# Kernel tuning notes

Measured on AMD Instinct MI355X. Metric: run time of the kernel, lower is better.

The kernel has to match this reference:

```python
import jax, jax.numpy as jnp
import numpy as np

D_MODEL = 1024
NUM_HEADS = 16
D_K = D_MODEL // NUM_HEADS
THETA = 10000.0


def _rope(x, cos, sin):
    # x: [b, h, l, d_k]; cos/sin: [l, d_k//2]
    x1 = x[..., ::2]
    x2 = x[..., 1::2]
    re = x1 * cos - x2 * sin
    ro = x1 * sin + x2 * cos
    return jnp.stack([re, ro], axis=-1).reshape(x.shape)


def setup_inputs() -> dict:
    key = jax.random.key(0)
    k0, k1, k2, k3, k4 = jax.random.split(key, 5)
    b, l = 2, 2048
    scale = 1.0 / np.sqrt(D_MODEL)
    return {
        "in_features": jax.random.normal(k0, (b, l, D_MODEL), dtype=jnp.float32),
        "wq": jax.random.normal(k1, (D_MODEL, D_MODEL), dtype=jnp.float32) * scale,
        "wk": jax.random.normal(k2, (D_MODEL, D_MODEL), dtype=jnp.float32) * scale,
        "wv": jax.random.normal(k3, (D_MODEL, D_MODEL), dtype=jnp.float32) * scale,
        "wo": jax.random.normal(k4, (D_MODEL, D_MODEL), dtype=jnp.float32) * scale,
    }


def reference(in_features, wq, wk, wv, wo):
    b, l, d = in_features.shape
    h, dk = NUM_HEADS, D_K

    def proj(w):
        # torch: einsum('b l d, k d -> b l k') == x @ w.T
        y = jnp.einsum('bld,kd->blk', in_features, w)
        return y.reshape(b, l, h, dk).transpose(0, 2, 1, 3)  # [b,h,l,dk]

    Q, K, V = proj(wq), proj(wk), proj(wv)

    # RoPE (use_rope=True)
    inv_freq = 1.0 / (THETA ** (jnp.arange(0, dk, 2, dtype=jnp.float32) / dk))
    angles = jnp.arange(l, dtype=jnp.float32)[:, None] * inv_freq[None, :]  # [l, dk//2]
    cos, sin = jnp.cos(angles), jnp.sin(angles)
    Q = _rope(Q, cos, sin)
    K = _rope(K, cos, sin)

    scores = jnp.einsum('bhqd,bhkd->bhqk', Q, K) / jnp.sqrt(jnp.float32(dk))
    causal = jnp.tril(jnp.ones((l, l), dtype=bool))  # [l,l]
    scores = jnp.where(causal[None, None], scores, jnp.float32(-jnp.inf))
    attn = jax.nn.softmax(scores, axis=-1)
    ctx = jnp.einsum('bhqk,bhkd->bhqd', attn, V)
    ctx = ctx.transpose(0, 2, 1, 3).reshape(b, l, d)  # [b,l,d_model]
    out = jnp.einsum('bld,md->blm', ctx, wo)
    return out
```

## Files before the change

### kernel.cpp

```cpp
#include <hip/hip_runtime.h>
#include <stdint.h>

typedef __attribute__((ext_vector_type(8))) short short8;
typedef __attribute__((ext_vector_type(4))) float floatx4;
typedef __attribute__((ext_vector_type(16))) float floatx16;

#define DEV static __device__ __forceinline__

DEV unsigned short f2bf(float f) {
  union { float f; uint32_t u; } v; v.f = f;
  return (unsigned short)((v.u + 0x7FFFu + ((v.u >> 16) & 1u)) >> 16);
}
DEV float bf2f(unsigned short h) {
  union { uint32_t u; float f; } v; v.u = ((uint32_t)h) << 16;
  return v.f;
}
DEV uint32_t cvtpk(float lo, float hi) {
  uint32_t d;
  asm("v_cvt_pk_bf16_f32 %0, %1, %2" : "=v"(d) : "v"(lo), "v"(hi));
  return d;
}
DEV void gload_lds16(const void* g, void* l) {
  __builtin_amdgcn_global_load_lds(
      (const __attribute__((address_space(1))) uint32_t*)g,
      (__attribute__((address_space(3))) uint32_t*)l, 16, 0, 0);
}

#if defined(__has_builtin)
#if __has_builtin(__builtin_amdgcn_permlane32_swap)
#define HAVE_PLSWAP 1
#endif
#endif
DEV void plswap(uint32_t& a, uint32_t& b) {
#ifdef HAVE_PLSWAP
  typedef unsigned int u2v __attribute__((ext_vector_type(2)));
  u2v r = __builtin_amdgcn_permlane32_swap(a, b, false, false);
  a = r.x; b = r.y;
#else
  uint32_t sa = (uint32_t)__shfl_xor((int)a, 32);
  uint32_t sb = (uint32_t)__shfl_xor((int)b, 32);
  uint32_t lane = __lane_id();
  uint32_t na = lane < 32 ? a : sb;
  uint32_t nb = lane < 32 ? sa : b;
  a = na; b = nb;
#endif
}
DEV float xmax32(float x) {
  union { float f; uint32_t u; } a, b; a.f = x; b.f = x;
  plswap(a.u, b.u);
  return fmaxf(a.f, b.f);
}
DEV float xsum32(float x) {
  union { float f; uint32_t u; } a, b; a.f = x; b.f = x;
  plswap(a.u, b.u);
  return a.f + b.f;
}

__global__ __launch_bounds__(256) void k_convert(
    const float* __restrict__ X, const float* __restrict__ Wq,
    const float* __restrict__ Wk, const float* __restrict__ Wv,
    const float* __restrict__ Wo, unsigned short* __restrict__ out) {
  long gid = (long)blockIdx.x * 256 + threadIdx.x;
  long e = gid * 8;
  int seg = (int)(e >> 20);
  const float* src; long base;
  if (seg < 4)      { src = X;  base = 0; }
  else if (seg == 4){ src = Wq; base = 4l << 20; }
  else if (seg == 5){ src = Wk; base = 5l << 20; }
  else if (seg == 6){ src = Wv; base = 6l << 20; }
  else              { src = Wo; base = 7l << 20; }
  const float4* s4 = (const float4*)(src + (e - base));
  float4 a = s4[0], b = s4[1];
  union { uint4 q; unsigned short s[8]; } u;
  u.s[0] = f2bf(a.x); u.s[1] = f2bf(a.y); u.s[2] = f2bf(a.z); u.s[3] = f2bf(a.w);
  u.s[4] = f2bf(b.x); u.s[5] = f2bf(b.y); u.s[6] = f2bf(b.z); u.s[7] = f2bf(b.w);
  *(uint4*)(out + e) = u.q;
}

template <int MODE>
__global__ __launch_bounds__(256) void k_gemm(
    const unsigned short* __restrict__ A,
    const unsigned short* __restrict__ B0, const unsigned short* __restrict__ B1,
    const unsigned short* __restrict__ B2,
    unsigned short* __restrict__ Qo, unsigned short* __restrict__ Ko,
    unsigned short* __restrict__ VFo, float* __restrict__ Cf, int K) {
  constexpr int MI = (MODE == 1) ? 2 : 4;
  constexpr int BM = MI * 32;
  __shared__ unsigned short At[BM * 64];
  __shared__ unsigned short Bt[128 * 64];
  const int tid = threadIdx.x, lane = tid & 63, wid = tid >> 6;
  const int wm = (wid >> 1) * (MI * 16), wn = (wid & 1) * 64;
  const int g = lane >> 4, c0 = lane & 15;
  const int bm0 = blockIdx.x * BM;
  const int bnG = blockIdx.y * 128;
  const unsigned short* Bp;
  int bn0;
  if constexpr (MODE == 0) {
    int wsel = bnG >> 10;
    Bp = wsel == 0 ? B0 : (wsel == 1 ? B1 : B2);
    bn0 = bnG & 1023;
  } else { Bp = B0; bn0 = bnG; }
  floatx4 acc[MI][4] = {};
  const int nk = K >> 6;
  const int koff = (blockIdx.x + blockIdx.y * 3) & (nk - 1);
  const int swzr = (c0 & 7) << 4;
  for (int s = 0; s < nk; ++s) {
    const int kt = ((s + koff) & (nk - 1)) << 6;
#pragma unroll
    for (int i = 0; i < MI; ++i) {
      int o = tid * 16 + i * 4096;
      int row = o >> 7;
      int col = (o & 127) ^ ((row & 7) << 4);
      gload_lds16((const char*)A + ((long)(bm0 + row) * K + kt + (col >> 1)) * 2, (char*)At + o);
    }
#pragma unroll
    for (int i = 0; i < 4; ++i) {
      int o = tid * 16 + i * 4096;
      int row = o >> 7;
      int col = (o & 127) ^ ((row & 7) << 4);
      gload_lds16((const char*)Bp + ((long)(bn0 + row) * K + kt + (col >> 1)) * 2, (char*)Bt + o);
    }
    __syncthreads();
#pragma unroll
    for (int kk = 0; kk < 2; ++kk) {
      const int kb = kk * 64 + g * 16;
      short8 av[MI], bv[4];
#pragma unroll
      for (int mi = 0; mi < MI; ++mi)
        av[mi] = *(const short8*)((const char*)At + (wm + mi * 16 + c0) * 128 + (kb ^ swzr));
#pragma unroll
      for (int ni = 0; ni < 4; ++ni)
        bv[ni] = *(const short8*)((const char*)Bt + (wn + ni * 16 + c0) * 128 + (kb ^ swzr));
#pragma unroll
      for (int mi = 0; mi < MI; ++mi)
#pragma unroll
        for (int ni = 0; ni < 4; ++ni)
          acc[mi][ni] = __builtin_amdgcn_mfma_f32_16x16x32_bf16(av[mi], bv[ni], acc[mi][ni], 0, 0, 0);
    }
    __syncthreads();
  }
  if constexpr (MODE == 1) {
#pragma unroll
    for (int mi = 0; mi < MI; ++mi)
#pragma unroll
      for (int ni = 0; ni < 4; ++ni)
#pragma unroll
        for (int i = 0; i < 4; ++i) {
          int r = bm0 + wm + mi * 16 + 4 * g + i;
          int cg = bnG + wn + ni * 16 + c0;
          Cf[(long)r * 1024 + cg] = acc[mi][ni][i];
        }
  } else {
    const int wsel = bnG >> 10;
#pragma unroll
    for (int mi = 0; mi < MI; ++mi)
#pragma unroll
      for (int ni = 0; ni < 4; ++ni)
#pragma unroll
        for (int i = 0; i < 4; ++i) {
          int r = bm0 + wm + mi * 16 + 4 * g + i;
          int cg = bnG + wn + ni * 16 + c0;
          int cc = cg & 1023, head = cc >> 6, dkk = cc & 63;
          int bb = r >> 11, ll = r & 2047;
          long bh = bb * 16 + head;
          float v = acc[mi][ni][i];
          if (wsel == 2) {
            int T = ll >> 6, rt = ll & 63;
            int m = rt >> 4, hb = (rt >> 3) & 1, j = rt & 7;
            int dvs = dkk >> 5, c = dkk & 31;
            VFo[bh * 131072 + T * 4096 + (dvs * 4 + m) * 512 + (hb * 32 + c) * 8 + j] = f2bf(v);
          } else {
            unsigned short* dst = wsel == 0 ? Qo : Ko;
            dst[(bh * 2048 + ll) * 64 + dkk] = f2bf(v);
          }
        }
  }
}

__global__ __launch_bounds__(256) void k_ropeQK(
    unsigned short* __restrict__ Qd, const unsigned short* __restrict__ Kin,
    unsigned short* __restrict__ KF, float qscale) {
  const int blk = blockIdx.x;
  const int tid = threadIdx.x;
  if (blk < 512) {
    int gid = blk * 256 + tid;
    int row = gid >> 1, hf = gid & 1;
    int l = row & 2047;
    unsigned short* p = Qd + (long)row * 64 + hf * 32;
    union { uint4 q[4]; unsigned short s[32]; } u;
#pragma unroll
    for (int i = 0; i < 4; ++i) u.q[i] = ((const uint4*)p)[i];
    float lf = (float)l;
#pragma unroll
    for (int j = 0; j < 16; ++j) {
      int pp = hf * 16 + j;
      float ang = lf * exp2f(-(float)pp * 0.4152410118609203f);
      float sv, cv; sincosf(ang, &sv, &cv);
      float x1 = bf2f(u.s[2 * j]), x2 = bf2f(u.s[2 * j + 1]);
      u.s[2 * j]     = f2bf((x1 * cv - x2 * sv) * qscale);
      u.s[2 * j + 1] = f2bf((x1 * sv + x2 * cv) * qscale);
    }
#pragma unroll
    for (int i = 0; i < 4; ++i) ((uint4*)p)[i] = u.q[i];
  } else {
    const int kblk = blk - 512;
    const int bh = kblk >> 5, T = kblk & 31;
    const unsigned short* src = Kin + ((long)bh * 2048 + T * 64) * 64;
    unsigned short* dst = KF + (long)kblk * 4096;
#pragma unroll
    for (int it = 0; it < 2; ++it) {
      int u = tid + it * 256;
      int lane = u & 63, kd = u >> 6;
      int kvs = kd >> 2, dseg = kd & 3;
      int row = kvs * 32 + (lane & 31);
      int col = dseg * 16 + 8 * (lane >> 5);
      union { uint4 q; unsigned short s[8]; } v;
      v.q = *(const uint4*)(src + row * 64 + col);
      float lf = (float)(T * 64 + row);
#pragma unroll
      for (int j = 0; j < 4; ++j) {
        int p = (col >> 1) + j;
        float ang = lf * exp2f(-(float)p * 0.4152410118609203f);
        float sv, cv; sincosf(ang, &sv, &cv);
        float x1 = bf2f(v.s[2 * j]), x2 = bf2f(v.s[2 * j + 1]);
        v.s[2 * j]     = f2bf(x1 * cv - x2 * sv);
        v.s[2 * j + 1] = f2bf(x1 * sv + x2 * cv);
      }
      *(uint4*)(dst + u * 8) = v.q;
    }
  }
}

DEV void attn_tile(int T, int Tend, int ntm1, int qabs, int h, int c,
                   const unsigned short* __restrict__ kfbase,
                   const unsigned short* __restrict__ vfbase,
                   const short8 (&qf)[4],
                   const short8 (&kc0)[4], const short8 (&kc1)[4],
                   short8 (&kn0)[4], short8 (&kn1)[4],
                   floatx16& ctx0, floatx16& ctx1, float& m_, float& l_) {
  {
    const int Tn = T + 1 < Tend ? T + 1 : T;
    const unsigned short* kt = kfbase + (long)Tn * 4096;
#pragma unroll
    for (int d = 0; d < 4; ++d) kn0[d] = *(const short8*)(kt + d * 512);
#pragma unroll
    for (int d = 0; d < 4; ++d) kn1[d] = *(const short8*)(kt + 2048 + d * 512);
  }
  const unsigned short* vt = vfbase + (long)T * 4096;
  short8 vf0[4], vf1[4];
#pragma unroll
  for (int m = 0; m < 4; ++m) vf0[m] = *(const short8*)(vt + m * 512);
#pragma unroll
  for (int m = 0; m < 4; ++m) vf1[m] = *(const short8*)(vt + 2048 + m * 512);

  floatx16 s0 = {}, s1 = {};
#pragma unroll
  for (int d = 0; d < 4; ++d)
    s0 = __builtin_amdgcn_mfma_f32_32x32x16_bf16(kc0[d], qf[d], s0, 0, 0, 0);
#pragma unroll
  for (int d = 0; d < 4; ++d)
    s1 = __builtin_amdgcn_mfma_f32_32x32x16_bf16(kc1[d], qf[d], s1, 0, 0, 0);

  if (T == ntm1) {
    const int kvb = T * 64 + 4 * h;
#pragma unroll
    for (int r = 0; r < 16; ++r) {
      const int off = (r & 3) + 8 * (r >> 2);
      if (kvb + off > qabs) s0[r] = -1e30f;
      if (kvb + 32 + off > qabs) s1[r] = -1e30f;
    }
  }
  float a4[8];
#pragma unroll
  for (int j = 0; j < 4; ++j) {
    a4[j]     = fmaxf(fmaxf(s0[4 * j], s0[4 * j + 1]), fmaxf(s0[4 * j + 2], s0[4 * j + 3]));
    a4[4 + j] = fmaxf(fmaxf(s1[4 * j], s1[4 * j + 1]), fmaxf(s1[4 * j + 2], s1[4 * j + 3]));
  }
  float mx = fmaxf(fmaxf(fmaxf(a4[0], a4[1]), fmaxf(a4[2], a4[3])),
                   fmaxf(fmaxf(a4[4], a4[5]), fmaxf(a4[6], a4[7])));
  mx = xmax32(mx);
  if (!__all(mx <= m_ + 8.0f)) {
    float mn = fmaxf(m_, mx);
    float sc = exp2f(m_ - mn);
    m_ = mn;
    l_ *= sc;
#pragma unroll
    for (int r = 0; r < 16; ++r) { ctx0[r] *= sc; ctx1[r] *= sc; }
  }
#pragma unroll
  for (int r = 0; r < 16; ++r) s0[r] = exp2f(s0[r] - m_);
#pragma unroll
  for (int r = 0; r < 16; ++r) s1[r] = exp2f(s1[r] - m_);
  float b4[8];
#pragma unroll
  for (int j = 0; j < 4; ++j) {
    b4[j]     = (s0[4 * j] + s0[4 * j + 1]) + (s0[4 * j + 2] + s0[4 * j + 3]);
    b4[4 + j] = (s1[4 * j] + s1[4 * j + 1]) + (s1[4 * j + 2] + s1[4 * j + 3]);
  }
  float rs = ((b4[0] + b4[1]) + (b4[2] + b4[3])) + ((b4[4] + b4[5]) + (b4[6] + b4[7]));
  rs = xsum32(rs);
  l_ += rs;

  uint32_t pd0[8], pd1[8];
#pragma unroll
  for (int d = 0; d < 8; ++d) {
    pd0[d] = cvtpk(s0[2 * d], s0[2 * d + 1]);
    pd1[d] = cvtpk(s1[2 * d], s1[2 * d + 1]);
  }
#pragma unroll
  for (int kvs = 0; kvs < 2; ++kvs) {
    const uint32_t* pd = kvs ? pd1 : pd0;
#pragma unroll
    for (int ks = 0; ks < 2; ++ks) {
      uint32_t u0 = pd[4 * ks], u2 = pd[4 * ks + 2];
      uint32_t u1 = pd[4 * ks + 1], u3 = pd[4 * ks + 3];
      plswap(u0, u2);
      plswap(u1, u3);
      union { uint32_t u[4]; short8 s; } bu;
      bu.u[0] = u0; bu.u[1] = u1; bu.u[2] = u2; bu.u[3] = u3;
      ctx0 = __builtin_amdgcn_mfma_f32_32x32x16_bf16(vf0[kvs * 2 + ks], bu.s, ctx0, 0, 0, 0);
      ctx1 = __builtin_amdgcn_mfma_f32_32x32x16_bf16(vf1[kvs * 2 + ks], bu.s, ctx1, 0, 0, 0);
    }
  }
}

__global__ __launch_bounds__(128) void k_attn(
    const unsigned short* __restrict__ Q, const unsigned short* __restrict__ KF,
    const unsigned short* __restrict__ VF, unsigned short* __restrict__ O) {
  __shared__ float lctx[64][33];
  __shared__ float lml[64][2];
  const int bid = blockIdx.x;
  const int xcd = bid & 7, idx = bid >> 3;
  const int head = idx >> 6;
  const int a = idx & 63;
  const int qs = (head < 2) ? a : 63 - a;
  const int bh = xcd * 4 + head;
  const int tid = threadIdx.x;
  const int wid = tid >> 6, lane = tid & 63;
  const int h = lane >> 5, c = lane & 31;
  const unsigned short* Qh = Q + (long)bh * 2048 * 64;
  const unsigned short* kfbase = KF + (long)bh * 131072 + lane * 8;
  const unsigned short* vfbase = VF + (long)bh * 131072 + lane * 8;
  const int q0 = qs * 32, qabs = q0 + c;
  const int nt = (qs >> 1) + 1, ntm1 = nt - 1;
  const int h0 = nt >> 1;
  const int Tbeg = wid ? h0 : 0;
  const int Tend = wid ? nt : h0;

  short8 qf[4];
#pragma unroll
  for (int d = 0; d < 4; ++d)
    qf[d] = *(const short8*)(Qh + (long)(q0 + c) * 64 + d * 16 + 8 * h);

  floatx16 ctx0 = {}, ctx1 = {};
  float m_ = -1e30f, l_ = 0.f;

  if (Tbeg < Tend) {
    short8 kA0[4], kA1[4], kB0[4], kB1[4];
    const unsigned short* kt0 = kfbase + (long)Tbeg * 4096;
#pragma unroll
    for (int d = 0; d < 4; ++d) kA0[d] = *(const short8*)(kt0 + d * 512);
#pragma unroll
    for (int d = 0; d < 4; ++d) kA1[d] = *(const short8*)(kt0 + 2048 + d * 512);
    int T = Tbeg;
    while (true) {
      attn_tile(T, Tend, ntm1, qabs, h, c, kfbase, vfbase, qf, kA0, kA1, kB0, kB1, ctx0, ctx1, m_, l_);
      if (++T >= Tend) break;
      attn_tile(T, Tend, ntm1, qabs, h, c, kfbase, vfbase, qf, kB0, kB1, kA0, kA1, ctx0, ctx1, m_, l_);
      if (++T >= Tend) break;
    }
  }
  if (wid) {
#pragma unroll
    for (int r = 0; r < 16; ++r) {
      lctx[lane][r] = ctx0[r];
      lctx[lane][16 + r] = ctx1[r];
    }
    lml[lane][0] = m_;
    lml[lane][1] = l_;
  }
  __syncthreads();
  if (!wid) {
    float m1 = lml[lane][0], l1 = lml[lane][1];
    float m = fmaxf(m_, m1);
    float e0 = exp2f(m_ - m), e1 = exp2f(m1 - m);
    float inv = 1.f / (l_ * e0 + l1 * e1);
    const int b = bh >> 4, hd = bh & 15;
    unsigned short* orow = O + (long)(b * 2048 + q0 + c) * 1024 + hd * 64;
#pragma unroll
    for (int m4 = 0; m4 < 4; ++m4) {
      uint2 w0, w1;
      w0.x = cvtpk((ctx0[4 * m4]     * e0 + lctx[lane][4 * m4]     * e1) * inv,
                   (ctx0[4 * m4 + 1] * e0 + lctx[lane][4 * m4 + 1] * e1) * inv);
      w0.y = cvtpk((ctx0[4 * m4 + 2] * e0 + lctx[lane][4 * m4 + 2] * e1) * inv,
                   (ctx0[4 * m4 + 3] * e0 + lctx[lane][4 * m4 + 3] * e1) * inv);
      *(uint2*)(orow + 8 * m4 + 4 * h) = w0;
      w1.x = cvtpk((ctx1[4 * m4]     * e0 + lctx[lane][16 + 4 * m4]     * e1) * inv,
                   (ctx1[4 * m4 + 1] * e0 + lctx[lane][16 + 4 * m4 + 1] * e1) * inv);
      w1.y = cvtpk((ctx1[4 * m4 + 2] * e0 + lctx[lane][16 + 4 * m4 + 2] * e1) * inv,
                   (ctx1[4 * m4 + 3] * e0 + lctx[lane][16 + 4 * m4 + 3] * e1) * inv);
      *(uint2*)(orow + 32 + 8 * m4 + 4 * h) = w1;
    }
  }
}

extern "C" void kernel_launch(void* const* d_in, const int* in_sizes, int n_in,
                              void* d_out, int out_size, void* d_ws, size_t ws_size,
                              hipStream_t stream) {
  const float* X  = (const float*)d_in[0];
  const float* Wq = (const float*)d_in[1];
  const float* Wk = (const float*)d_in[2];
  const float* Wv = (const float*)d_in[3];
  const float* Wo = (const float*)d_in[4];
  unsigned short* Xb  = (unsigned short*)d_ws;
  unsigned short* Wqb = Xb + (4l << 20);
  unsigned short* Wkb = Xb + (5l << 20);
  unsigned short* Wvb = Xb + (6l << 20);
  unsigned short* Wob = Xb + (7l << 20);
  unsigned short* Qw  = Xb + (8l << 20);
  unsigned short* Kw  = Xb + (12l << 20);
  unsigned short* VFw = Xb + (16l << 20);
  unsigned short* KFw = Xb;
  unsigned short* Cw  = Xb + (20l << 20);
  float* Out = (float*)d_out;

  k_convert<<<4096, 256, 0, stream>>>(X, Wq, Wk, Wv, Wo, Xb);
  k_gemm<0><<<dim3(32, 24), 256, 0, stream>>>(Xb, Wqb, Wkb, Wvb, Qw, Kw, VFw, nullptr, 1024);
  k_ropeQK<<<1536, 256, 0, stream>>>(Qw, Kw, KFw, 0.18033688011112042f);
  k_attn<<<2048, 128, 0, stream>>>(Qw, KFw, VFw, Cw);
  k_gemm<1><<<dim3(64, 8), 256, 0, stream>>>(Cw, Wob, nullptr, nullptr,
                                             nullptr, nullptr, nullptr, Out, 1024);
}
```

Before: 128.0 us.

## Process two KV tiles per softmax step and add MFMA priority hints

```diff
diff --git a/kernel.cpp b/kernel.cpp
--- a/kernel.cpp
+++ b/kernel.cpp
@@ -231,82 +231,10 @@
   }
 }
 
-DEV void attn_tile(int T, int Tend, int ntm1, int qabs, int h, int c,
-                   const unsigned short* __restrict__ kfbase,
-                   const unsigned short* __restrict__ vfbase,
-                   const short8 (&qf)[4],
-                   const short8 (&kc0)[4], const short8 (&kc1)[4],
-                   short8 (&kn0)[4], short8 (&kn1)[4],
-                   floatx16& ctx0, floatx16& ctx1, float& m_, float& l_) {
-  {
-    const int Tn = T + 1 < Tend ? T + 1 : T;
-    const unsigned short* kt = kfbase + (long)Tn * 4096;
-#pragma unroll
-    for (int d = 0; d < 4; ++d) kn0[d] = *(const short8*)(kt + d * 512);
-#pragma unroll
-    for (int d = 0; d < 4; ++d) kn1[d] = *(const short8*)(kt + 2048 + d * 512);
-  }
-  const unsigned short* vt = vfbase + (long)T * 4096;
-  short8 vf0[4], vf1[4];
-#pragma unroll
-  for (int m = 0; m < 4; ++m) vf0[m] = *(const short8*)(vt + m * 512);
-#pragma unroll
-  for (int m = 0; m < 4; ++m) vf1[m] = *(const short8*)(vt + 2048 + m * 512);
-
-  floatx16 s0 = {}, s1 = {};
-#pragma unroll
-  for (int d = 0; d < 4; ++d)
-    s0 = __builtin_amdgcn_mfma_f32_32x32x16_bf16(kc0[d], qf[d], s0, 0, 0, 0);
-#pragma unroll
-  for (int d = 0; d < 4; ++d)
-    s1 = __builtin_amdgcn_mfma_f32_32x32x16_bf16(kc1[d], qf[d], s1, 0, 0, 0);
-
-  if (T == ntm1) {
-    const int kvb = T * 64 + 4 * h;
-#pragma unroll
-    for (int r = 0; r < 16; ++r) {
-      const int off = (r & 3) + 8 * (r >> 2);
-      if (kvb + off > qabs) s0[r] = -1e30f;
-      if (kvb + 32 + off > qabs) s1[r] = -1e30f;
-    }
-  }
-  float a4[8];
-#pragma unroll
-  for (int j = 0; j < 4; ++j) {
-    a4[j]     = fmaxf(fmaxf(s0[4 * j], s0[4 * j + 1]), fmaxf(s0[4 * j + 2], s0[4 * j + 3]));
-    a4[4 + j] = fmaxf(fmaxf(s1[4 * j], s1[4 * j + 1]), fmaxf(s1[4 * j + 2], s1[4 * j + 3]));
-  }
-  float mx = fmaxf(fmaxf(fmaxf(a4[0], a4[1]), fmaxf(a4[2], a4[3])),
-                   fmaxf(fmaxf(a4[4], a4[5]), fmaxf(a4[6], a4[7])));
-  mx = xmax32(mx);
-  if (!__all(mx <= m_ + 8.0f)) {
-    float mn = fmaxf(m_, mx);
-    float sc = exp2f(m_ - mn);
-    m_ = mn;
-    l_ *= sc;
-#pragma unroll
-    for (int r = 0; r < 16; ++r) { ctx0[r] *= sc; ctx1[r] *= sc; }
-  }
-#pragma unroll
-  for (int r = 0; r < 16; ++r) s0[r] = exp2f(s0[r] - m_);
-#pragma unroll
-  for (int r = 0; r < 16; ++r) s1[r] = exp2f(s1[r] - m_);
-  float b4[8];
-#pragma unroll
-  for (int j = 0; j < 4; ++j) {
-    b4[j]     = (s0[4 * j] + s0[4 * j + 1]) + (s0[4 * j + 2] + s0[4 * j + 3]);
-    b4[4 + j] = (s1[4 * j] + s1[4 * j + 1]) + (s1[4 * j + 2] + s1[4 * j + 3]);
-  }
-  float rs = ((b4[0] + b4[1]) + (b4[2] + b4[3])) + ((b4[4] + b4[5]) + (b4[6] + b4[7]));
-  rs = xsum32(rs);
-  l_ += rs;
-
-  uint32_t pd0[8], pd1[8];
-#pragma unroll
-  for (int d = 0; d < 8; ++d) {
-    pd0[d] = cvtpk(s0[2 * d], s0[2 * d + 1]);
-    pd1[d] = cvtpk(s1[2 * d], s1[2 * d + 1]);
-  }
+
+DEV void pv_tile(const uint32_t (&pd0)[8], const uint32_t (&pd1)[8],
+                 const short8 (&vf0)[4], const short8 (&vf1)[4],
+                 floatx16& ctx0, floatx16& ctx1) {
 #pragma unroll
   for (int kvs = 0; kvs < 2; ++kvs) {
     const uint32_t* pd = kvs ? pd1 : pd0;
@@ -322,6 +250,170 @@
       ctx1 = __builtin_amdgcn_mfma_f32_32x32x16_bf16(vf1[kvs * 2 + ks], bu.s, ctx1, 0, 0, 0);
     }
   }
+}
+
+DEV void mask_tile(int kvb, int qabs, floatx16& s0, floatx16& s1) {
+#pragma unroll
+  for (int r = 0; r < 16; ++r) {
+    const int off = (r & 3) + 8 * (r >> 2);
+    if (kvb + off > qabs) s0[r] = -1e30f;
+    if (kvb + 32 + off > qabs) s1[r] = -1e30f;
+  }
+}
+
+DEV void attn_tile2(int T, int ntm1, int qabs, int h,
+                    const unsigned short* __restrict__ kfbase,
+                    const unsigned short* __restrict__ vfbase,
+                    const short8 (&qf)[4],
+                    floatx16& ctx0, floatx16& ctx1, float& m_, float& l_) {
+  const unsigned short* ktA = kfbase + (long)T * 4096;
+  short8 kA0[4], kA1[4], kB0[4], kB1[4];
+#pragma unroll
+  for (int d = 0; d < 4; ++d) {
+    kA0[d] = *(const short8*)(ktA + d * 512);
+    kA1[d] = *(const short8*)(ktA + 2048 + d * 512);
+    kB0[d] = *(const short8*)(ktA + 4096 + d * 512);
+    kB1[d] = *(const short8*)(ktA + 6144 + d * 512);
+  }
+  floatx16 sA0 = {}, sA1 = {}, sB0 = {}, sB1 = {};
+  __builtin_amdgcn_s_setprio(1);
+#pragma unroll
+  for (int d = 0; d < 4; ++d) {
+    sA0 = __builtin_amdgcn_mfma_f32_32x32x16_bf16(kA0[d], qf[d], sA0, 0, 0, 0);
+    sA1 = __builtin_amdgcn_mfma_f32_32x32x16_bf16(kA1[d], qf[d], sA1, 0, 0, 0);
+    sB0 = __builtin_amdgcn_mfma_f32_32x32x16_bf16(kB0[d], qf[d], sB0, 0, 0, 0);
+    sB1 = __builtin_amdgcn_mfma_f32_32x32x16_bf16(kB1[d], qf[d], sB1, 0, 0, 0);
+  }
+  __builtin_amdgcn_s_setprio(0);
+  const unsigned short* vtA = vfbase + (long)T * 4096;
+  short8 vA0[4], vA1[4], vB0[4], vB1[4];
+#pragma unroll
+  for (int m = 0; m < 4; ++m) {
+    vA0[m] = *(const short8*)(vtA + m * 512);
+    vA1[m] = *(const short8*)(vtA + 2048 + m * 512);
+    vB0[m] = *(const short8*)(vtA + 4096 + m * 512);
+    vB1[m] = *(const short8*)(vtA + 6144 + m * 512);
+  }
+  if (T + 1 == ntm1) mask_tile((T + 1) * 64 + 4 * h, qabs, sB0, sB1);
+  float a8[8];
+#pragma unroll
+  for (int j = 0; j < 4; ++j) {
+    a8[j] = fmaxf(fmaxf(fmaxf(sA0[4 * j], sA0[4 * j + 1]), fmaxf(sA0[4 * j + 2], sA0[4 * j + 3])),
+                  fmaxf(fmaxf(sA1[4 * j], sA1[4 * j + 1]), fmaxf(sA1[4 * j + 2], sA1[4 * j + 3])));
+    a8[4 + j] = fmaxf(fmaxf(fmaxf(sB0[4 * j], sB0[4 * j + 1]), fmaxf(sB0[4 * j + 2], sB0[4 * j + 3])),
+                      fmaxf(fmaxf(sB1[4 * j], sB1[4 * j + 1]), fmaxf(sB1[4 * j + 2], sB1[4 * j + 3])));
+  }
+  float mx = fmaxf(fmaxf(fmaxf(a8[0], a8[1]), fmaxf(a8[2], a8[3])),
+                   fmaxf(fmaxf(a8[4], a8[5]), fmaxf(a8[6], a8[7])));
+  mx = xmax32(mx);
+  if (!__all(mx <= m_ + 8.0f)) {
+    float mn = fmaxf(m_, mx);
+    float sc = exp2f(m_ - mn);
+    m_ = mn;
+    l_ *= sc;
+#pragma unroll
+    for (int r = 0; r < 16; ++r) { ctx0[r] *= sc; ctx1[r] *= sc; }
+  }
+#pragma unroll
+  for (int r = 0; r < 16; ++r) {
+    sA0[r] = exp2f(sA0[r] - m_);
+    sA1[r] = exp2f(sA1[r] - m_);
+    sB0[r] = exp2f(sB0[r] - m_);
+    sB1[r] = exp2f(sB1[r] - m_);
+  }
+  float rs = 0.f;
+#pragma unroll
+  for (int j = 0; j < 4; ++j) {
+    float t0 = (sA0[4 * j] + sA0[4 * j + 1]) + (sA0[4 * j + 2] + sA0[4 * j + 3]);
+    float t1 = (sA1[4 * j] + sA1[4 * j + 1]) + (sA1[4 * j + 2] + sA1[4 * j + 3]);
+    float t2 = (sB0[4 * j] + sB0[4 * j + 1]) + (sB0[4 * j + 2] + sB0[4 * j + 3]);
+    float t3 = (sB1[4 * j] + sB1[4 * j + 1]) + (sB1[4 * j + 2] + sB1[4 * j + 3]);
+    rs += (t0 + t1) + (t2 + t3);
+  }
+  rs = xsum32(rs);
+  l_ += rs;
+  uint32_t pA0[8], pA1[8], pB0[8], pB1[8];
+#pragma unroll
+  for (int d = 0; d < 8; ++d) {
+    pA0[d] = cvtpk(sA0[2 * d], sA0[2 * d + 1]);
+    pA1[d] = cvtpk(sA1[2 * d], sA1[2 * d + 1]);
+    pB0[d] = cvtpk(sB0[2 * d], sB0[2 * d + 1]);
+    pB1[d] = cvtpk(sB1[2 * d], sB1[2 * d + 1]);
+  }
+  __builtin_amdgcn_s_setprio(1);
+  pv_tile(pA0, pA1, vA0, vA1, ctx0, ctx1);
+  pv_tile(pB0, pB1, vB0, vB1, ctx0, ctx1);
+  __builtin_amdgcn_s_setprio(0);
+}
+
+DEV void attn_tile1(int T, int ntm1, int qabs, int h,
+                    const unsigned short* __restrict__ kfbase,
+                    const unsigned short* __restrict__ vfbase,
+                    const short8 (&qf)[4],
+                    floatx16& ctx0, floatx16& ctx1, float& m_, float& l_) {
+  const unsigned short* kt = kfbase + (long)T * 4096;
+  short8 k0[4], k1[4];
+#pragma unroll
+  for (int d = 0; d < 4; ++d) {
+    k0[d] = *(const short8*)(kt + d * 512);
+    k1[d] = *(const short8*)(kt + 2048 + d * 512);
+  }
+  floatx16 s0 = {}, s1 = {};
+  __builtin_amdgcn_s_setprio(1);
+#pragma unroll
+  for (int d = 0; d < 4; ++d) {
+    s0 = __builtin_amdgcn_mfma_f32_32x32x16_bf16(k0[d], qf[d], s0, 0, 0, 0);
+    s1 = __builtin_amdgcn_mfma_f32_32x32x16_bf16(k1[d], qf[d], s1, 0, 0, 0);
+  }
+  __builtin_amdgcn_s_setprio(0);
+  const unsigned short* vt = vfbase + (long)T * 4096;
+  short8 vf0[4], vf1[4];
+#pragma unroll
+  for (int m = 0; m < 4; ++m) {
+    vf0[m] = *(const short8*)(vt + m * 512);
+    vf1[m] = *(const short8*)(vt + 2048 + m * 512);
+  }
+  if (T == ntm1) mask_tile(T * 64 + 4 * h, qabs, s0, s1);
+  float a4[8];
+#pragma unroll
+  for (int j = 0; j < 4; ++j) {
+    a4[j]     = fmaxf(fmaxf(s0[4 * j], s0[4 * j + 1]), fmaxf(s0[4 * j + 2], s0[4 * j + 3]));
+    a4[4 + j] = fmaxf(fmaxf(s1[4 * j], s1[4 * j + 1]), fmaxf(s1[4 * j + 2], s1[4 * j + 3]));
+  }
+  float mx = fmaxf(fmaxf(fmaxf(a4[0], a4[1]), fmaxf(a4[2], a4[3])),
+                   fmaxf(fmaxf(a4[4], a4[5]), fmaxf(a4[6], a4[7])));
+  mx = xmax32(mx);
+  if (!__all(mx <= m_ + 8.0f)) {
+    float mn = fmaxf(m_, mx);
+    float sc = exp2f(m_ - mn);
+    m_ = mn;
+    l_ *= sc;
+#pragma unroll
+    for (int r = 0; r < 16; ++r) { ctx0[r] *= sc; ctx1[r] *= sc; }
+  }
+#pragma unroll
+  for (int r = 0; r < 16; ++r) {
+    s0[r] = exp2f(s0[r] - m_);
+    s1[r] = exp2f(s1[r] - m_);
+  }
+  float rs = 0.f;
+#pragma unroll
+  for (int j = 0; j < 4; ++j) {
+    float t0 = (s0[4 * j] + s0[4 * j + 1]) + (s0[4 * j + 2] + s0[4 * j + 3]);
+    float t1 = (s1[4 * j] + s1[4 * j + 1]) + (s1[4 * j + 2] + s1[4 * j + 3]);
+    rs += t0 + t1;
+  }
+  rs = xsum32(rs);
+  l_ += rs;
+  uint32_t pd0[8], pd1[8];
+#pragma unroll
+  for (int d = 0; d < 8; ++d) {
+    pd0[d] = cvtpk(s0[2 * d], s0[2 * d + 1]);
+    pd1[d] = cvtpk(s1[2 * d], s1[2 * d + 1]);
+  }
+  __builtin_amdgcn_s_setprio(1);
+  pv_tile(pd0, pd1, vf0, vf1, ctx0, ctx1);
+  __builtin_amdgcn_s_setprio(0);
 }
 
 __global__ __launch_bounds__(128) void k_attn(
@@ -355,21 +447,15 @@
   floatx16 ctx0 = {}, ctx1 = {};
   float m_ = -1e30f, l_ = 0.f;
 
-  if (Tbeg < Tend) {
-    short8 kA0[4], kA1[4], kB0[4], kB1[4];
-    const unsigned short* kt0 = kfbase + (long)Tbeg * 4096;
-#pragma unroll
-    for (int d = 0; d < 4; ++d) kA0[d] = *(const short8*)(kt0 + d * 512);
-#pragma unroll
-    for (int d = 0; d < 4; ++d) kA1[d] = *(const short8*)(kt0 + 2048 + d * 512);
-    int T = Tbeg;
-    while (true) {
-      attn_tile(T, Tend, ntm1, qabs, h, c, kfbase, vfbase, qf, kA0, kA1, kB0, kB1, ctx0, ctx1, m_, l_);
-      if (++T >= Tend) break;
-      attn_tile(T, Tend, ntm1, qabs, h, c, kfbase, vfbase, qf, kB0, kB1, kA0, kA1, ctx0, ctx1, m_, l_);
-      if (++T >= Tend) break;
-    }
-  }
+  int T = Tbeg;
+#pragma unroll 1
+  while (T + 1 < Tend) {
+    attn_tile2(T, ntm1, qabs, h, kfbase, vfbase, qf, ctx0, ctx1, m_, l_);
+    T += 2;
+  }
+  if (T < Tend)
+    attn_tile1(T, ntm1, qabs, h, kfbase, vfbase, qf, ctx0, ctx1, m_, l_);
+
   if (wid) {
 #pragma unroll
     for (int r = 0; r < 16; ++r) {
```

After: 132.7 us. 1.04x slower.
